# Kernel optimization log

Measured on AMD Instinct MI355X. Metric: run time of the kernel, lower is better.

Reference implementation:

```python
import itertools
import jax, jax.numpy as jnp
import numpy as np

B, O, E = 4096, 8, 64        # batch, num objects, latent dim
I, V = 4, 3                  # max_invariants, max_variables
PERM_IDXS = np.array(list(itertools.permutations(range(O), V)), dtype=np.int32)  # [P, V], P = 8*7*6 = 336


def setup_inputs() -> dict:
    key = jax.random.key(0)
    k1, k2, k3, k4 = jax.random.split(key, 4)
    return {
        "unary_feats": jax.random.normal(k1, (B, O, E), dtype=jnp.float32),
        "binary_feats": jax.random.normal(k2, (B, O, O, E), dtype=jnp.float32),
        # learned weights (RandomNormal(mean=0) in the original, stddev 0.05 default)
        "rule_unary": jax.random.normal(k3, (I, V, E), dtype=jnp.float32) * 0.05,
        "rule_binary": jax.random.normal(k4, (I, V, V, E), dtype=jnp.float32) * 0.05,
    }


def reference(unary_feats, binary_feats, rule_unary, rule_binary):
    perm = jnp.asarray(PERM_IDXS)  # [P, V]
    # unary_match[b,i,k,l] = sum_e unary_feats[b,l,e] * rule_unary[i,k,e]
    unary_match = jnp.einsum('ble,ike->bikl', unary_feats, rule_unary)  # [B, I, V, O]
    # gather: unary_perm_scores[b,i,p,v] = unary_match[b,i,v,perm[p,v]]
    v_idx = jnp.arange(V)[None, :]                      # [1, V]
    unary_perm_scores = unary_match[:, :, v_idx, perm]  # [B, I, P, V]
    unary_scores = unary_perm_scores.sum(-1)            # [B, I, P]

    # binary_match[b,i,n,m,j,k] = sum_e binary_feats[b,j,k,e] * rule_binary[i,n,m,e]
    binary_match = jnp.einsum('bjke,inme->binmjk', binary_feats, rule_binary)  # [B, I, V, V, O, O]
    # gather per permutation: scores[b,i,p,n,m] = binary_match[b,i,n,m,perm[p,n],perm[p,m]]
    n = jnp.arange(V)[None, :, None]  # [1, V, 1]
    m = jnp.arange(V)[None, None, :]  # [1, 1, V]
    pn = perm[:, :, None]             # [P, V, 1]
    pm = perm[:, None, :]             # [P, 1, V]
    binary_perm_scores = binary_match[:, :, n, m, pn, pm]  # [B, I, P, V, V]
    binary_scores = binary_perm_scores.sum((-1, -2))        # [B, I, P]

    merged_scores = (unary_scores + binary_scores).min(-1)  # [B, I] (min over permutations)
    inv_select = jax.nn.softmax(merged_scores, axis=-1)     # [B, I]
    rule_labels = jax.nn.one_hot(jnp.array([0, 0, 1, 1]), 4, dtype=inv_select.dtype)  # [4, 4]
    return inv_select @ rule_labels                          # [B, 4]
```

## Files before the change

kernel.cpp:

```cpp
#include <hip/hip_runtime.h>
#include <math.h>


typedef __attribute__((ext_vector_type(8))) __bf16 bf16x8;
typedef __attribute__((ext_vector_type(4))) float  f32x4;

#define BMS 68
#define QS3 68

__device__ inline bf16x8 cvt2(const float4 v0, const float4 v1) {
    bf16x8 r;
    r[0] = (__bf16)v0.x; r[1] = (__bf16)v0.y; r[2] = (__bf16)v0.z; r[3] = (__bf16)v0.w;
    r[4] = (__bf16)v1.x; r[5] = (__bf16)v1.y; r[6] = (__bf16)v1.z; r[7] = (__bf16)v1.w;
    return r;
}

__global__ __launch_bounds__(64, 2) void rule_learner_kernel(
    const float* __restrict__ uf,
    const float* __restrict__ bfe,
    const float* __restrict__ ru,
    const float* __restrict__ rb,
    float* __restrict__ out)
{
    const int b0    = blockIdx.x * 2;
    const int lane  = threadIdx.x;
    const int row16 = lane & 15;
    const int kg    = lane >> 4;
    const int kb    = kg * 8;

    __shared__ float bm[36 * BMS];
    __shared__ float um[12 * 12];
    __shared__ float q [12 * QS3];

    float4 af[4][4], uA[4];
    {
        const float* base = bfe + (size_t)b0 * 4096;
        #pragma unroll
        for (int t = 0; t < 4; ++t) {
            const float* rp = base + (size_t)(t * 16 + row16) * 64 + kb;
            af[t][0] = *(const float4*)rp;
            af[t][1] = *(const float4*)(rp + 4);
            af[t][2] = *(const float4*)(rp + 32);
            af[t][3] = *(const float4*)(rp + 36);
        }
        const float* up = uf + (size_t)b0 * 512 + (row16 < 8 ? row16 : 7) * 64 + kb;
        uA[0] = *(const float4*)up;
        uA[1] = *(const float4*)(up + 4);
        uA[2] = *(const float4*)(up + 32);
        uA[3] = *(const float4*)(up + 36);
    }

    bf16x8 rbf[6], ruf0, ruf1;
    {
        #pragma unroll
        for (int nt = 0; nt < 3; ++nt) {
            const int rule = nt * 16 + row16;
            const float* rp = rb + (rule < 36 ? rule : 35) * 64 + kb;
            rbf[nt * 2 + 0] = cvt2(*(const float4*)rp,        *(const float4*)(rp + 4));
            rbf[nt * 2 + 1] = cvt2(*(const float4*)(rp + 32), *(const float4*)(rp + 36));
        }
        const float* up = ru + (row16 < 12 ? row16 : 11) * 64 + kb;
        ruf0 = cvt2(*(const float4*)up,        *(const float4*)(up + 4));
        ruf1 = cvt2(*(const float4*)(up + 32), *(const float4*)(up + 36));
    }

    #pragma unroll
    for (int e = 0; e < 2; ++e) {
        #pragma unroll
        for (int t = 0; t < 4; ++t) {
            const bf16x8 a0 = cvt2(af[t][0], af[t][1]);
            const bf16x8 a1 = cvt2(af[t][2], af[t][3]);
            #pragma unroll
            for (int nt = 0; nt < 3; ++nt) {
                f32x4 acc = {0.f, 0.f, 0.f, 0.f};
                acc = __builtin_amdgcn_mfma_f32_16x16x32_bf16(a0, rbf[nt * 2 + 0], acc, 0, 0, 0);
                acc = __builtin_amdgcn_mfma_f32_16x16x32_bf16(a1, rbf[nt * 2 + 1], acc, 0, 0, 0);
                const int rule = nt * 16 + row16;
                if (rule < 36)
                    *(float4*)&bm[rule * BMS + t * 16 + kg * 4] = *(float4*)&acc;
            }
        }
        {
            const bf16x8 ua0 = cvt2(uA[0], uA[1]);
            const bf16x8 ua1 = cvt2(uA[2], uA[3]);
            f32x4 acc = {0.f, 0.f, 0.f, 0.f};
            acc = __builtin_amdgcn_mfma_f32_16x16x32_bf16(ua0, ruf0, acc, 0, 0, 0);
            acc = __builtin_amdgcn_mfma_f32_16x16x32_bf16(ua1, ruf1, acc, 0, 0, 0);
            if (row16 < 12 && kg < 2)
                *(float4*)&um[row16 * 12 + kg * 4] = *(float4*)&acc;
        }

        if (e == 0) {
            const float* base = bfe + (size_t)(b0 + 1) * 4096;
            #pragma unroll
            for (int t = 0; t < 4; ++t) {
                const float* rp = base + (size_t)(t * 16 + row16) * 64 + kb;
                af[t][0] = *(const float4*)rp;
                af[t][1] = *(const float4*)(rp + 4);
                af[t][2] = *(const float4*)(rp + 32);
                af[t][3] = *(const float4*)(rp + 36);
            }
            const float* up = uf + (size_t)(b0 + 1) * 512
                            + (row16 < 8 ? row16 : 7) * 64 + kb;
            uA[0] = *(const float4*)up;
            uA[1] = *(const float4*)(up + 4);
            uA[2] = *(const float4*)(up + 32);
            uA[3] = *(const float4*)(up + 36);
        }

        {
            const int x = lane >> 3;
            const int y = lane & 7;
            #pragma unroll
            for (int i = 0; i < 4; ++i) {
                const float* bmi = bm + i * 9 * BMS;
                const float* umi = um + i * 3 * 12;
                const float q01 = umi[x] + umi[12 + y]
                                + bmi[0 * BMS + x * 9] + bmi[4 * BMS + y * 9]
                                + bmi[1 * BMS + x * 8 + y] + bmi[3 * BMS + y * 8 + x];
                const float q02 = umi[24 + y] + bmi[8 * BMS + y * 9]
                                + bmi[2 * BMS + x * 8 + y] + bmi[6 * BMS + y * 8 + x];
                const float q12 = bmi[5 * BMS + x * 8 + y] + bmi[7 * BMS + y * 8 + x];
                q[(i * 3 + 0) * QS3 + lane] = q01;
                q[(i * 3 + 1) * QS3 + lane] = q02;
                q[(i * 3 + 2) * QS3 + lane] = q12;
            }
        }

        float mn[4] = {INFINITY, INFINITY, INFINITY, INFINITY};
        if (lane < 56) {
            const int a  = lane / 7;
            const int o  = lane - a * 7;
            const int bb = o + (o >= a);
            #pragma unroll
            for (int i = 0; i < 4; ++i) {
                const float bs  = q[(i * 3 + 0) * QS3 + a * 8 + bb];
                const float4 c0 = *(const float4*)&q[(i * 3 + 1) * QS3 + a * 8];
                const float4 c1 = *(const float4*)&q[(i * 3 + 1) * QS3 + a * 8 + 4];
                const float4 d0 = *(const float4*)&q[(i * 3 + 2) * QS3 + bb * 8];
                const float4 d1 = *(const float4*)&q[(i * 3 + 2) * QS3 + bb * 8 + 4];
                float vv[8];
                vv[0] = c0.x + d0.x; vv[1] = c0.y + d0.y;
                vv[2] = c0.z + d0.z; vv[3] = c0.w + d0.w;
                vv[4] = c1.x + d1.x; vv[5] = c1.y + d1.y;
                vv[6] = c1.z + d1.z; vv[7] = c1.w + d1.w;
                float m = INFINITY;
                #pragma unroll
                for (int cc = 0; cc < 8; ++cc) {
                    const float s = (cc == a || cc == bb) ? INFINITY : (bs + vv[cc]);
                    m = fminf(m, s);
                }
                mn[i] = m;
            }
        }
        #pragma unroll
        for (int s = 1; s <= 32; s <<= 1) {
            #pragma unroll
            for (int i = 0; i < 4; ++i) mn[i] = fminf(mn[i], __shfl_xor(mn[i], s));
        }
        if (lane == 0) {
            const float mx = fmaxf(fmaxf(mn[0], mn[1]), fmaxf(mn[2], mn[3]));
            const float e0 = expf(mn[0] - mx), e1 = expf(mn[1] - mx);
            const float e2 = expf(mn[2] - mx), e3 = expf(mn[3] - mx);
            const float inv = 1.f / (e0 + e1 + e2 + e3);
            *(float4*)(out + (size_t)(b0 + e) * 4) =
                make_float4((e0 + e1) * inv, (e2 + e3) * inv, 0.f, 0.f);
        }

        if (e == 0) {
            asm volatile("s_waitcnt lgkmcnt(0)" ::: "memory");
            __builtin_amdgcn_sched_barrier(0);
        }
    }
}

extern "C" void kernel_launch(void* const* d_in, const int* in_sizes, int n_in,
                              void* d_out, int out_size, void* d_ws, size_t ws_size,
                              hipStream_t stream) {
    const float* uf = (const float*)d_in[0];
    const float* bf = (const float*)d_in[1];
    const float* ru = (const float*)d_in[2];
    const float* rb = (const float*)d_in[3];
    float* out = (float*)d_out;

    const int B = in_sizes[0] / (8 * 64);
    rule_learner_kernel<<<B / 2, 64, 0, stream>>>(uf, bf, ru, rb, out);
}
```

Before: 20.66 us.

## Cut binary MFMAs by folding rule pairs and diagonal terms into fewer GEMMs

The kernel no longer computes all 36 rule-by-pair binary matches. It computes only the off-diagonal rule pairs needed for each (i,pair) slot, two rule sets of 12 columns each, and adds the transposed partner from shared memory. The diagonal binary terms are merged into the unary MFMA by loading the diagonal binary_feats rows. This reduces MFMA count and shared-memory traffic, and it drops the separate q-assembly pass, at the cost of extra diagonal loads and a strided transposed LDS gather.

```diff
diff --git a/kernel.cpp b/kernel.cpp
--- a/kernel.cpp
+++ b/kernel.cpp
@@ -5,8 +5,8 @@
 typedef __attribute__((ext_vector_type(8))) __bf16 bf16x8;
 typedef __attribute__((ext_vector_type(4))) float  f32x4;
 
-#define BMS 68
-#define QS3 68
+#define QS 68
+#define SS 12
 
 __device__ inline bf16x8 cvt2(const float4 v0, const float4 v1) {
     bf16x8 r;
@@ -28,11 +28,32 @@
     const int kg    = lane >> 4;
     const int kb    = kg * 8;
 
-    __shared__ float bm[36 * BMS];
-    __shared__ float um[12 * 12];
-    __shared__ float q [12 * QS3];
-
-    float4 af[4][4], uA[4];
+    __shared__ float q_s [12 * QS];
+    __shared__ float q2_s[12 * QS];
+    __shared__ float ss_s[12 * SS];
+
+    const int cc16  = row16 < 12 ? row16 : 11;
+    const int ii    = cc16 / 3, tt = cc16 - ii * 3;
+    const int rule1 = ii * 9 + (tt == 0 ? 1 : tt == 1 ? 2 : 5);
+    const int rule2 = ii * 9 + (tt == 0 ? 3 : tt == 1 ? 6 : 7);
+    const int ruled = ii * 9 + tt * 4;
+    bf16x8 b1f0, b1f1, b2f0, b2f1, dbf0, dbf1, ruf0, ruf1;
+    {
+        const float* r1 = rb + rule1 * 64 + kb;
+        b1f0 = cvt2(*(const float4*)r1,        *(const float4*)(r1 + 4));
+        b1f1 = cvt2(*(const float4*)(r1 + 32), *(const float4*)(r1 + 36));
+        const float* r2 = rb + rule2 * 64 + kb;
+        b2f0 = cvt2(*(const float4*)r2,        *(const float4*)(r2 + 4));
+        b2f1 = cvt2(*(const float4*)(r2 + 32), *(const float4*)(r2 + 36));
+        const float* rd = rb + ruled * 64 + kb;
+        dbf0 = cvt2(*(const float4*)rd,        *(const float4*)(rd + 4));
+        dbf1 = cvt2(*(const float4*)(rd + 32), *(const float4*)(rd + 36));
+        const float* rr = ru + cc16 * 64 + kb;
+        ruf0 = cvt2(*(const float4*)rr,        *(const float4*)(rr + 4));
+        ruf1 = cvt2(*(const float4*)(rr + 32), *(const float4*)(rr + 36));
+    }
+
+    float4 af[4][4], uA[4], dA[4];
     {
         const float* base = bfe + (size_t)b0 * 4096;
         #pragma unroll
@@ -43,51 +64,44 @@
             af[t][2] = *(const float4*)(rp + 32);
             af[t][3] = *(const float4*)(rp + 36);
         }
-        const float* up = uf + (size_t)b0 * 512 + (row16 < 8 ? row16 : 7) * 64 + kb;
-        uA[0] = *(const float4*)up;
-        uA[1] = *(const float4*)(up + 4);
-        uA[2] = *(const float4*)(up + 32);
-        uA[3] = *(const float4*)(up + 36);
-    }
-
-    bf16x8 rbf[6], ruf0, ruf1;
-    {
-        #pragma unroll
-        for (int nt = 0; nt < 3; ++nt) {
-            const int rule = nt * 16 + row16;
-            const float* rp = rb + (rule < 36 ? rule : 35) * 64 + kb;
-            rbf[nt * 2 + 0] = cvt2(*(const float4*)rp,        *(const float4*)(rp + 4));
-            rbf[nt * 2 + 1] = cvt2(*(const float4*)(rp + 32), *(const float4*)(rp + 36));
-        }
-        const float* up = ru + (row16 < 12 ? row16 : 11) * 64 + kb;
-        ruf0 = cvt2(*(const float4*)up,        *(const float4*)(up + 4));
-        ruf1 = cvt2(*(const float4*)(up + 32), *(const float4*)(up + 36));
+        const int v8c = row16 < 8 ? row16 : 7;
+        const float* up = uf + (size_t)b0 * 512 + v8c * 64 + kb;
+        uA[0] = *(const float4*)up;        uA[1] = *(const float4*)(up + 4);
+        uA[2] = *(const float4*)(up + 32); uA[3] = *(const float4*)(up + 36);
+        const float* dp = base + v8c * 576 + kb;
+        dA[0] = *(const float4*)dp;        dA[1] = *(const float4*)(dp + 4);
+        dA[2] = *(const float4*)(dp + 32); dA[3] = *(const float4*)(dp + 36);
     }
 
     #pragma unroll
     for (int e = 0; e < 2; ++e) {
+        f32x4 g1[4];
         #pragma unroll
         for (int t = 0; t < 4; ++t) {
             const bf16x8 a0 = cvt2(af[t][0], af[t][1]);
             const bf16x8 a1 = cvt2(af[t][2], af[t][3]);
-            #pragma unroll
-            for (int nt = 0; nt < 3; ++nt) {
-                f32x4 acc = {0.f, 0.f, 0.f, 0.f};
-                acc = __builtin_amdgcn_mfma_f32_16x16x32_bf16(a0, rbf[nt * 2 + 0], acc, 0, 0, 0);
-                acc = __builtin_amdgcn_mfma_f32_16x16x32_bf16(a1, rbf[nt * 2 + 1], acc, 0, 0, 0);
-                const int rule = nt * 16 + row16;
-                if (rule < 36)
-                    *(float4*)&bm[rule * BMS + t * 16 + kg * 4] = *(float4*)&acc;
-            }
+            f32x4 z1 = {0.f, 0.f, 0.f, 0.f};
+            z1 = __builtin_amdgcn_mfma_f32_16x16x32_bf16(a0, b1f0, z1, 0, 0, 0);
+            z1 = __builtin_amdgcn_mfma_f32_16x16x32_bf16(a1, b1f1, z1, 0, 0, 0);
+            g1[t] = z1;
+            f32x4 z2 = {0.f, 0.f, 0.f, 0.f};
+            z2 = __builtin_amdgcn_mfma_f32_16x16x32_bf16(a0, b2f0, z2, 0, 0, 0);
+            z2 = __builtin_amdgcn_mfma_f32_16x16x32_bf16(a1, b2f1, z2, 0, 0, 0);
+            if (row16 < 12)
+                *(float4*)&q2_s[row16 * QS + t * 16 + kg * 4] = *(float4*)&z2;
         }
         {
             const bf16x8 ua0 = cvt2(uA[0], uA[1]);
             const bf16x8 ua1 = cvt2(uA[2], uA[3]);
-            f32x4 acc = {0.f, 0.f, 0.f, 0.f};
-            acc = __builtin_amdgcn_mfma_f32_16x16x32_bf16(ua0, ruf0, acc, 0, 0, 0);
-            acc = __builtin_amdgcn_mfma_f32_16x16x32_bf16(ua1, ruf1, acc, 0, 0, 0);
+            const bf16x8 da0 = cvt2(dA[0], dA[1]);
+            const bf16x8 da1 = cvt2(dA[2], dA[3]);
+            f32x4 zs = {0.f, 0.f, 0.f, 0.f};
+            zs = __builtin_amdgcn_mfma_f32_16x16x32_bf16(ua0, ruf0, zs, 0, 0, 0);
+            zs = __builtin_amdgcn_mfma_f32_16x16x32_bf16(ua1, ruf1, zs, 0, 0, 0);
+            zs = __builtin_amdgcn_mfma_f32_16x16x32_bf16(da0, dbf0, zs, 0, 0, 0);
+            zs = __builtin_amdgcn_mfma_f32_16x16x32_bf16(da1, dbf1, zs, 0, 0, 0);
             if (row16 < 12 && kg < 2)
-                *(float4*)&um[row16 * 12 + kg * 4] = *(float4*)&acc;
+                *(float4*)&ss_s[row16 * SS + kg * 4] = *(float4*)&zs;
         }
 
         if (e == 0) {
@@ -100,30 +114,40 @@
                 af[t][2] = *(const float4*)(rp + 32);
                 af[t][3] = *(const float4*)(rp + 36);
             }
-            const float* up = uf + (size_t)(b0 + 1) * 512
-                            + (row16 < 8 ? row16 : 7) * 64 + kb;
-            uA[0] = *(const float4*)up;
-            uA[1] = *(const float4*)(up + 4);
-            uA[2] = *(const float4*)(up + 32);
-            uA[3] = *(const float4*)(up + 36);
-        }
-
-        {
-            const int x = lane >> 3;
-            const int y = lane & 7;
-            #pragma unroll
-            for (int i = 0; i < 4; ++i) {
-                const float* bmi = bm + i * 9 * BMS;
-                const float* umi = um + i * 3 * 12;
-                const float q01 = umi[x] + umi[12 + y]
-                                + bmi[0 * BMS + x * 9] + bmi[4 * BMS + y * 9]
-                                + bmi[1 * BMS + x * 8 + y] + bmi[3 * BMS + y * 8 + x];
-                const float q02 = umi[24 + y] + bmi[8 * BMS + y * 9]
-                                + bmi[2 * BMS + x * 8 + y] + bmi[6 * BMS + y * 8 + x];
-                const float q12 = bmi[5 * BMS + x * 8 + y] + bmi[7 * BMS + y * 8 + x];
-                q[(i * 3 + 0) * QS3 + lane] = q01;
-                q[(i * 3 + 1) * QS3 + lane] = q02;
-                q[(i * 3 + 2) * QS3 + lane] = q12;
+            const int v8c = row16 < 8 ? row16 : 7;
+            const float* up = uf + (size_t)(b0 + 1) * 512 + v8c * 64 + kb;
+            uA[0] = *(const float4*)up;        uA[1] = *(const float4*)(up + 4);
+            uA[2] = *(const float4*)(up + 32); uA[3] = *(const float4*)(up + 36);
+            const float* dp = base + v8c * 576 + kb;
+            dA[0] = *(const float4*)dp;        dA[1] = *(const float4*)(dp + 4);
+            dA[2] = *(const float4*)(dp + 32); dA[3] = *(const float4*)(dp + 36);
+        }
+
+        if (row16 < 12) {
+            #pragma unroll
+            for (int t = 0; t < 4; ++t) {
+                const int p0 = t * 16 + kg * 4;
+                float4 add;
+                {
+                    const int p = p0 + 0, rv = ((p & 7) << 3) | (p >> 3);
+                    add.x = q2_s[row16 * QS + rv];
+                }
+                {
+                    const int p = p0 + 1, rv = ((p & 7) << 3) | (p >> 3);
+                    add.y = q2_s[row16 * QS + rv];
+                }
+                {
+                    const int p = p0 + 2, rv = ((p & 7) << 3) | (p >> 3);
+                    add.z = q2_s[row16 * QS + rv];
+                }
+                {
+                    const int p = p0 + 3, rv = ((p & 7) << 3) | (p >> 3);
+                    add.w = q2_s[row16 * QS + rv];
+                }
+                float4 res;
+                res.x = g1[t][0] + add.x; res.y = g1[t][1] + add.y;
+                res.z = g1[t][2] + add.z; res.w = g1[t][3] + add.w;
+                *(float4*)&q_s[row16 * QS + p0] = res;
             }
         }
 
@@ -134,16 +158,20 @@
             const int bb = o + (o >= a);
             #pragma unroll
             for (int i = 0; i < 4; ++i) {
-                const float bs  = q[(i * 3 + 0) * QS3 + a * 8 + bb];
-                const float4 c0 = *(const float4*)&q[(i * 3 + 1) * QS3 + a * 8];
-                const float4 c1 = *(const float4*)&q[(i * 3 + 1) * QS3 + a * 8 + 4];
-                const float4 d0 = *(const float4*)&q[(i * 3 + 2) * QS3 + bb * 8];
-                const float4 d1 = *(const float4*)&q[(i * 3 + 2) * QS3 + bb * 8 + 4];
+                const float bs = q_s[(i * 3 + 0) * QS + a * 8 + bb]
+                               + ss_s[(i * 3 + 0) * SS + a]
+                               + ss_s[(i * 3 + 1) * SS + bb];
+                const float4 c0 = *(const float4*)&q_s[(i * 3 + 1) * QS + a * 8];
+                const float4 c1 = *(const float4*)&q_s[(i * 3 + 1) * QS + a * 8 + 4];
+                const float4 d0 = *(const float4*)&q_s[(i * 3 + 2) * QS + bb * 8];
+                const float4 d1 = *(const float4*)&q_s[(i * 3 + 2) * QS + bb * 8 + 4];
+                const float4 e0 = *(const float4*)&ss_s[(i * 3 + 2) * SS];
+                const float4 e1 = *(const float4*)&ss_s[(i * 3 + 2) * SS + 4];
                 float vv[8];
-                vv[0] = c0.x + d0.x; vv[1] = c0.y + d0.y;
-                vv[2] = c0.z + d0.z; vv[3] = c0.w + d0.w;
-                vv[4] = c1.x + d1.x; vv[5] = c1.y + d1.y;
-                vv[6] = c1.z + d1.z; vv[7] = c1.w + d1.w;
+                vv[0] = c0.x + d0.x + e0.x; vv[1] = c0.y + d0.y + e0.y;
+                vv[2] = c0.z + d0.z + e0.z; vv[3] = c0.w + d0.w + e0.w;
+                vv[4] = c1.x + d1.x + e1.x; vv[5] = c1.y + d1.y + e1.y;
+                vv[6] = c1.z + d1.z + e1.z; vv[7] = c1.w + d1.w + e1.w;
                 float m = INFINITY;
                 #pragma unroll
                 for (int cc = 0; cc < 8; ++cc) {
```

New measurement: 21.44 us. +3.8%, slower.

## Transpose binary match layout to pair-major and keep q01 in registers

Applied to the files above, without the earlier changes.

Swaps the MFMA operand order so binary match results are stored per object pair (64 rows) with rules permuted into a packed order. The q-assembly phase can then read contiguous float4/float2 vectors per lane instead of many scalar strided LDS loads. The q01 term stays in registers rather than going through shared memory, and the min phase uses all 64 lanes indexed directly by (x,y). The gain relies on getting the rule permutation and the LDS strides right, and there is a risk of LDS bank conflicts with the new stride of 52.

```diff
diff --git a/kernel.cpp b/kernel.cpp
--- a/kernel.cpp
+++ b/kernel.cpp
@@ -5,8 +5,9 @@
 typedef __attribute__((ext_vector_type(8))) __bf16 bf16x8;
 typedef __attribute__((ext_vector_type(4))) float  f32x4;
 
-#define BMS 68
-#define QS3 68
+#define BMS2 52
+#define QS2  68
+#define SSU  12
 
 __device__ inline bf16x8 cvt2(const float4 v0, const float4 v1) {
     bf16x8 r;
@@ -27,10 +28,30 @@
     const int row16 = lane & 15;
     const int kg    = lane >> 4;
     const int kb    = kg * 8;
+    const int x     = lane >> 3;
+    const int y     = lane & 7;
+    const int rev   = y * 8 + x;
 
-    __shared__ float bm[36 * BMS];
-    __shared__ float um[12 * 12];
-    __shared__ float q [12 * QS3];
+    __shared__ float bm_t[64 * BMS2];
+    __shared__ float q_s [8 * QS2];
+    __shared__ float um  [12 * SSU];
+
+    bf16x8 raf[6];
+    #pragma unroll
+    for (int T = 0; T < 3; ++T) {
+        const int c = T * 16 + row16;
+        const int i = c / 12, s = c - i * 12;
+        const int m = (int)((0x008407630521ull >> (4 * s)) & 15ull);
+        const float* rp = rb + (i * 9 + m) * 64 + kb;
+        raf[T * 2 + 0] = cvt2(*(const float4*)rp,        *(const float4*)(rp + 4));
+        raf[T * 2 + 1] = cvt2(*(const float4*)(rp + 32), *(const float4*)(rp + 36));
+    }
+    bf16x8 ruf0, ruf1;
+    {
+        const float* rr = ru + (row16 < 12 ? row16 : 11) * 64 + kb;
+        ruf0 = cvt2(*(const float4*)rr,        *(const float4*)(rr + 4));
+        ruf1 = cvt2(*(const float4*)(rr + 32), *(const float4*)(rr + 36));
+    }
 
     float4 af[4][4], uA[4];
     {
@@ -44,40 +65,22 @@
             af[t][3] = *(const float4*)(rp + 36);
         }
         const float* up = uf + (size_t)b0 * 512 + (row16 < 8 ? row16 : 7) * 64 + kb;
-        uA[0] = *(const float4*)up;
-        uA[1] = *(const float4*)(up + 4);
-        uA[2] = *(const float4*)(up + 32);
-        uA[3] = *(const float4*)(up + 36);
-    }
-
-    bf16x8 rbf[6], ruf0, ruf1;
-    {
-        #pragma unroll
-        for (int nt = 0; nt < 3; ++nt) {
-            const int rule = nt * 16 + row16;
-            const float* rp = rb + (rule < 36 ? rule : 35) * 64 + kb;
-            rbf[nt * 2 + 0] = cvt2(*(const float4*)rp,        *(const float4*)(rp + 4));
-            rbf[nt * 2 + 1] = cvt2(*(const float4*)(rp + 32), *(const float4*)(rp + 36));
-        }
-        const float* up = ru + (row16 < 12 ? row16 : 11) * 64 + kb;
-        ruf0 = cvt2(*(const float4*)up,        *(const float4*)(up + 4));
-        ruf1 = cvt2(*(const float4*)(up + 32), *(const float4*)(up + 36));
+        uA[0] = *(const float4*)up;        uA[1] = *(const float4*)(up + 4);
+        uA[2] = *(const float4*)(up + 32); uA[3] = *(const float4*)(up + 36);
     }
 
     #pragma unroll
-    for (int e = 0; e < 2; ++e) {
+    for (int el = 0; el < 2; ++el) {
         #pragma unroll
-        for (int t = 0; t < 4; ++t) {
-            const bf16x8 a0 = cvt2(af[t][0], af[t][1]);
-            const bf16x8 a1 = cvt2(af[t][2], af[t][3]);
+        for (int P = 0; P < 4; ++P) {
+            const bf16x8 fb0 = cvt2(af[P][0], af[P][1]);
+            const bf16x8 fb1 = cvt2(af[P][2], af[P][3]);
             #pragma unroll
-            for (int nt = 0; nt < 3; ++nt) {
+            for (int T = 0; T < 3; ++T) {
                 f32x4 acc = {0.f, 0.f, 0.f, 0.f};
-                acc = __builtin_amdgcn_mfma_f32_16x16x32_bf16(a0, rbf[nt * 2 + 0], acc, 0, 0, 0);
-                acc = __builtin_amdgcn_mfma_f32_16x16x32_bf16(a1, rbf[nt * 2 + 1], acc, 0, 0, 0);
-                const int rule = nt * 16 + row16;
-                if (rule < 36)
-                    *(float4*)&bm[rule * BMS + t * 16 + kg * 4] = *(float4*)&acc;
+                acc = __builtin_amdgcn_mfma_f32_16x16x32_bf16(raf[T * 2 + 0], fb0, acc, 0, 0, 0);
+                acc = __builtin_amdgcn_mfma_f32_16x16x32_bf16(raf[T * 2 + 1], fb1, acc, 0, 0, 0);
+                *(float4*)&bm_t[(P * 16 + row16) * BMS2 + T * 16 + kg * 4] = *(float4*)&acc;
             }
         }
         {
@@ -87,14 +90,14 @@
             acc = __builtin_amdgcn_mfma_f32_16x16x32_bf16(ua0, ruf0, acc, 0, 0, 0);
             acc = __builtin_amdgcn_mfma_f32_16x16x32_bf16(ua1, ruf1, acc, 0, 0, 0);
             if (row16 < 12 && kg < 2)
-                *(float4*)&um[row16 * 12 + kg * 4] = *(float4*)&acc;
+                *(float4*)&um[row16 * SSU + kg * 4] = *(float4*)&acc;
         }
 
-        if (e == 0) {
-            const float* base = bfe + (size_t)(b0 + 1) * 4096;
+        if (el == 0) {
+            const float* nb = bfe + (size_t)(b0 + 1) * 4096;
             #pragma unroll
             for (int t = 0; t < 4; ++t) {
-                const float* rp = base + (size_t)(t * 16 + row16) * 64 + kb;
+                const float* rp = nb + (size_t)(t * 16 + row16) * 64 + kb;
                 af[t][0] = *(const float4*)rp;
                 af[t][1] = *(const float4*)(rp + 4);
                 af[t][2] = *(const float4*)(rp + 32);
@@ -102,43 +105,34 @@
             }
             const float* up = uf + (size_t)(b0 + 1) * 512
                             + (row16 < 8 ? row16 : 7) * 64 + kb;
-            uA[0] = *(const float4*)up;
-            uA[1] = *(const float4*)(up + 4);
-            uA[2] = *(const float4*)(up + 32);
-            uA[3] = *(const float4*)(up + 36);
+            uA[0] = *(const float4*)up;        uA[1] = *(const float4*)(up + 4);
+            uA[2] = *(const float4*)(up + 32); uA[3] = *(const float4*)(up + 36);
         }
 
-        {
-            const int x = lane >> 3;
-            const int y = lane & 7;
-            #pragma unroll
-            for (int i = 0; i < 4; ++i) {
-                const float* bmi = bm + i * 9 * BMS;
-                const float* umi = um + i * 3 * 12;
-                const float q01 = umi[x] + umi[12 + y]
-                                + bmi[0 * BMS + x * 9] + bmi[4 * BMS + y * 9]
-                                + bmi[1 * BMS + x * 8 + y] + bmi[3 * BMS + y * 8 + x];
-                const float q02 = umi[24 + y] + bmi[8 * BMS + y * 9]
-                                + bmi[2 * BMS + x * 8 + y] + bmi[6 * BMS + y * 8 + x];
-                const float q12 = bmi[5 * BMS + x * 8 + y] + bmi[7 * BMS + y * 8 + x];
-                q[(i * 3 + 0) * QS3 + lane] = q01;
-                q[(i * 3 + 1) * QS3 + lane] = q02;
-                q[(i * 3 + 2) * QS3 + lane] = q12;
-            }
+        float q01r[4];
+        #pragma unroll
+        for (int i = 0; i < 4; ++i) {
+            const float4 F = *(const float4*)&bm_t[lane * BMS2 + i * 12];
+            const float4 R = *(const float4*)&bm_t[rev  * BMS2 + i * 12 + 4];
+            const float2 D = *(const float2*)&bm_t[(y * 9) * BMS2 + i * 12 + 8];
+            const float  z = bm_t[(x * 9) * BMS2 + i * 12 + 3];
+            const float u0 = um[(i * 3 + 0) * SSU + x];
+            const float u1 = um[(i * 3 + 1) * SSU + y];
+            const float u2 = um[(i * 3 + 2) * SSU + y];
+            q01r[i] = F.x + R.x + z + D.x + u0 + u1;
+            q_s[(i * 2 + 0) * QS2 + lane] = F.y + R.y + D.y + u2;
+            q_s[(i * 2 + 1) * QS2 + lane] = F.z + R.z;
         }
 
         float mn[4] = {INFINITY, INFINITY, INFINITY, INFINITY};
-        if (lane < 56) {
-            const int a  = lane / 7;
-            const int o  = lane - a * 7;
-            const int bb = o + (o >= a);
+        if (x != y) {
             #pragma unroll
             for (int i = 0; i < 4; ++i) {
-                const float bs  = q[(i * 3 + 0) * QS3 + a * 8 + bb];
-                const float4 c0 = *(const float4*)&q[(i * 3 + 1) * QS3 + a * 8];
-                const float4 c1 = *(const float4*)&q[(i * 3 + 1) * QS3 + a * 8 + 4];
-                const float4 d0 = *(const float4*)&q[(i * 3 + 2) * QS3 + bb * 8];
-                const float4 d1 = *(const float4*)&q[(i * 3 + 2) * QS3 + bb * 8 + 4];
+                const float  bs = q01r[i];
+                const float4 c0 = *(const float4*)&q_s[(i * 2 + 0) * QS2 + x * 8];
+                const float4 c1 = *(const float4*)&q_s[(i * 2 + 0) * QS2 + x * 8 + 4];
+                const float4 d0 = *(const float4*)&q_s[(i * 2 + 1) * QS2 + y * 8];
+                const float4 d1 = *(const float4*)&q_s[(i * 2 + 1) * QS2 + y * 8 + 4];
                 float vv[8];
                 vv[0] = c0.x + d0.x; vv[1] = c0.y + d0.y;
                 vv[2] = c0.z + d0.z; vv[3] = c0.w + d0.w;
@@ -147,7 +141,7 @@
                 float m = INFINITY;
                 #pragma unroll
                 for (int cc = 0; cc < 8; ++cc) {
-                    const float s = (cc == a || cc == bb) ? INFINITY : (bs + vv[cc]);
+                    const float s = (cc == x || cc == y) ? INFINITY : (bs + vv[cc]);
                     m = fminf(m, s);
                 }
                 mn[i] = m;
@@ -163,11 +157,11 @@
             const float e0 = expf(mn[0] - mx), e1 = expf(mn[1] - mx);
             const float e2 = expf(mn[2] - mx), e3 = expf(mn[3] - mx);
             const float inv = 1.f / (e0 + e1 + e2 + e3);
-            *(float4*)(out + (size_t)(b0 + e) * 4) =
+            *(float4*)(out + (size_t)(b0 + el) * 4) =
                 make_float4((e0 + e1) * inv, (e2 + e3) * inv, 0.f, 0.f);
         }
 
-        if (e == 0) {
+        if (el == 0) {
             asm volatile("s_waitcnt lgkmcnt(0)" ::: "memory");
             __builtin_amdgcn_sched_barrier(0);
         }
```

Measured after the change: 21.16 us. 2.5% more time.

## Process one batch per block and raise occupancy instead of manual prefetch

Applied to the files above, without the earlier changes.

Each block now handles a single batch element instead of two, so the grid doubles and the manual software prefetch of the second element goes away. Occupancy is raised by moving launch_bounds from 2 to 4 and by converting loaded inputs to bf16 immediately, which cuts live registers. Shared memory is shrunk by aliasing the q buffer onto the bm buffer and tightening the row strides. The aim is to hide the latency of the memory-bound binary-feature loads with more resident waves rather than explicit double-buffering. The cost is some extra per-block overhead, and the shared-memory aliasing is only safe because the kernel runs as a single wave.

```diff
diff --git a/kernel.cpp b/kernel.cpp
--- a/kernel.cpp
+++ b/kernel.cpp
@@ -5,8 +5,8 @@
 typedef __attribute__((ext_vector_type(8))) __bf16 bf16x8;
 typedef __attribute__((ext_vector_type(4))) float  f32x4;
 
-#define BMS 68
-#define QS3 68
+#define BMS 66
+#define SSU 12
 
 __device__ inline bf16x8 cvt2(const float4 v0, const float4 v1) {
     bf16x8 r;
@@ -15,39 +15,36 @@
     return r;
 }
 
-__global__ __launch_bounds__(64, 2) void rule_learner_kernel(
+__global__ __launch_bounds__(64, 4) void rule_learner_kernel(
     const float* __restrict__ uf,
     const float* __restrict__ bfe,
     const float* __restrict__ ru,
     const float* __restrict__ rb,
     float* __restrict__ out)
 {
-    const int b0    = blockIdx.x * 2;
+    const int b     = blockIdx.x;
     const int lane  = threadIdx.x;
     const int row16 = lane & 15;
     const int kg    = lane >> 4;
     const int kb    = kg * 8;
 
-    __shared__ float bm[36 * BMS];
-    __shared__ float um[12 * 12];
-    __shared__ float q [12 * QS3];
+    __shared__ float smem[36 * BMS + 12 * SSU];
+    float* bm = smem;
+    float* qq = smem;
+    float* um = smem + 36 * BMS;
 
-    float4 af[4][4], uA[4];
+    bf16x8 a0[4], a1[4], ua0, ua1;
     {
-        const float* base = bfe + (size_t)b0 * 4096;
+        const float* base = bfe + (size_t)b * 4096;
         #pragma unroll
         for (int t = 0; t < 4; ++t) {
             const float* rp = base + (size_t)(t * 16 + row16) * 64 + kb;
-            af[t][0] = *(const float4*)rp;
-            af[t][1] = *(const float4*)(rp + 4);
-            af[t][2] = *(const float4*)(rp + 32);
-            af[t][3] = *(const float4*)(rp + 36);
+            a0[t] = cvt2(*(const float4*)rp,        *(const float4*)(rp + 4));
+            a1[t] = cvt2(*(const float4*)(rp + 32), *(const float4*)(rp + 36));
         }
-        const float* up = uf + (size_t)b0 * 512 + (row16 < 8 ? row16 : 7) * 64 + kb;
-        uA[0] = *(const float4*)up;
-        uA[1] = *(const float4*)(up + 4);
-        uA[2] = *(const float4*)(up + 32);
-        uA[3] = *(const float4*)(up + 36);
+        const float* up = uf + (size_t)b * 512 + (row16 < 8 ? row16 : 7) * 64 + kb;
+        ua0 = cvt2(*(const float4*)up,        *(const float4*)(up + 4));
+        ua1 = cvt2(*(const float4*)(up + 32), *(const float4*)(up + 36));
     }
 
     bf16x8 rbf[6], ruf0, ruf1;
@@ -65,112 +62,83 @@
     }
 
     #pragma unroll
-    for (int e = 0; e < 2; ++e) {
+    for (int t = 0; t < 4; ++t) {
         #pragma unroll
-        for (int t = 0; t < 4; ++t) {
-            const bf16x8 a0 = cvt2(af[t][0], af[t][1]);
-            const bf16x8 a1 = cvt2(af[t][2], af[t][3]);
+        for (int nt = 0; nt < 3; ++nt) {
+            f32x4 acc = {0.f, 0.f, 0.f, 0.f};
+            acc = __builtin_amdgcn_mfma_f32_16x16x32_bf16(a0[t], rbf[nt * 2 + 0], acc, 0, 0, 0);
+            acc = __builtin_amdgcn_mfma_f32_16x16x32_bf16(a1[t], rbf[nt * 2 + 1], acc, 0, 0, 0);
+            const int rule = nt * 16 + row16;
+            if (rule < 36)
+                *(float4*)&bm[rule * BMS + t * 16 + kg * 4] = *(float4*)&acc;
+        }
+    }
+    {
+        f32x4 acc = {0.f, 0.f, 0.f, 0.f};
+        acc = __builtin_amdgcn_mfma_f32_16x16x32_bf16(ua0, ruf0, acc, 0, 0, 0);
+        acc = __builtin_amdgcn_mfma_f32_16x16x32_bf16(ua1, ruf1, acc, 0, 0, 0);
+        if (row16 < 12 && kg < 2)
+            *(float4*)&um[row16 * SSU + kg * 4] = *(float4*)&acc;
+    }
+
+    {
+        const int x = lane >> 3;
+        const int y = lane & 7;
+        #pragma unroll
+        for (int i = 0; i < 4; ++i) {
+            const float* bmi = bm + i * 9 * BMS;
+            const float* umi = um + i * 3 * SSU;
+            const float q01 = umi[x] + umi[SSU + y]
+                            + bmi[0 * BMS + x * 9] + bmi[4 * BMS + y * 9]
+                            + bmi[1 * BMS + x * 8 + y] + bmi[3 * BMS + y * 8 + x];
+            const float q02 = umi[2 * SSU + y] + bmi[8 * BMS + y * 9]
+                            + bmi[2 * BMS + x * 8 + y] + bmi[6 * BMS + y * 8 + x];
+            const float q12 = bmi[5 * BMS + x * 8 + y] + bmi[7 * BMS + y * 8 + x];
+            qq[(i * 3 + 0) * BMS + lane] = q01;
+            qq[(i * 3 + 1) * BMS + lane] = q02;
+            qq[(i * 3 + 2) * BMS + lane] = q12;
+        }
+    }
+
+    float mn[4] = {INFINITY, INFINITY, INFINITY, INFINITY};
+    if (lane < 56) {
+        const int a  = lane / 7;
+        const int o  = lane - a * 7;
+        const int bb = o + (o >= a);
+        #pragma unroll
+        for (int i = 0; i < 4; ++i) {
+            const float bs  = qq[(i * 3 + 0) * BMS + a * 8 + bb];
+            const float4 c0 = *(const float4*)&qq[(i * 3 + 1) * BMS + a * 8];
+            const float4 c1 = *(const float4*)&qq[(i * 3 + 1) * BMS + a * 8 + 4];
+            const float4 d0 = *(const float4*)&qq[(i * 3 + 2) * BMS + bb * 8];
+            const float4 d1 = *(const float4*)&qq[(i * 3 + 2) * BMS + bb * 8 + 4];
+            float vv[8];
+            vv[0] = c0.x + d0.x; vv[1] = c0.y + d0.y;
+            vv[2] = c0.z + d0.z; vv[3] = c0.w + d0.w;
+            vv[4] = c1.x + d1.x; vv[5] = c1.y + d1.y;
+            vv[6] = c1.z + d1.z; vv[7] = c1.w + d1.w;
+            float m = INFINITY;
             #pragma unroll
-            for (int nt = 0; nt < 3; ++nt) {
-                f32x4 acc = {0.f, 0.f, 0.f, 0.f};
-                acc = __builtin_amdgcn_mfma_f32_16x16x32_bf16(a0, rbf[nt * 2 + 0], acc, 0, 0, 0);
-                acc = __builtin_amdgcn_mfma_f32_16x16x32_bf16(a1, rbf[nt * 2 + 1], acc, 0, 0, 0);
-                const int rule = nt * 16 + row16;
-                if (rule < 36)
-                    *(float4*)&bm[rule * BMS + t * 16 + kg * 4] = *(float4*)&acc;
+            for (int cc = 0; cc < 8; ++cc) {
+                const float s = (cc == a || cc == bb) ? INFINITY : (bs + vv[cc]);
+                m = fminf(m, s);
             }
+            mn[i] = m;
         }
-        {
-            const bf16x8 ua0 = cvt2(uA[0], uA[1]);
-            const bf16x8 ua1 = cvt2(uA[2], uA[3]);
-            f32x4 acc = {0.f, 0.f, 0.f, 0.f};
-            acc = __builtin_amdgcn_mfma_f32_16x16x32_bf16(ua0, ruf0, acc, 0, 0, 0);
-            acc = __builtin_amdgcn_mfma_f32_16x16x32_bf16(ua1, ruf1, acc, 0, 0, 0);
-            if (row16 < 12 && kg < 2)
-                *(float4*)&um[row16 * 12 + kg * 4] = *(float4*)&acc;
-        }
+    }
+    #pragma unroll
+    for (int s = 1; s <= 32; s <<= 1) {
+        #pragma unroll
+        for (int i = 0; i < 4; ++i) mn[i] = fminf(mn[i], __shfl_xor(mn[i], s));
+    }
 
-        if (e == 0) {
-            const float* base = bfe + (size_t)(b0 + 1) * 4096;
-            #pragma unroll
-            for (int t = 0; t < 4; ++t) {
-                const float* rp = base + (size_t)(t * 16 + row16) * 64 + kb;
-                af[t][0] = *(const float4*)rp;
-                af[t][1] = *(const float4*)(rp + 4);
-                af[t][2] = *(const float4*)(rp + 32);
-                af[t][3] = *(const float4*)(rp + 36);
-            }
-            const float* up = uf + (size_t)(b0 + 1) * 512
-                            + (row16 < 8 ? row16 : 7) * 64 + kb;
-            uA[0] = *(const float4*)up;
-            uA[1] = *(const float4*)(up + 4);
-            uA[2] = *(const float4*)(up + 32);
-            uA[3] = *(const float4*)(up + 36);
-        }
-
-        {
-            const int x = lane >> 3;
-            const int y = lane & 7;
-            #pragma unroll
-            for (int i = 0; i < 4; ++i) {
-                const float* bmi = bm + i * 9 * BMS;
-                const float* umi = um + i * 3 * 12;
-                const float q01 = umi[x] + umi[12 + y]
-                                + bmi[0 * BMS + x * 9] + bmi[4 * BMS + y * 9]
-                                + bmi[1 * BMS + x * 8 + y] + bmi[3 * BMS + y * 8 + x];
-                const float q02 = umi[24 + y] + bmi[8 * BMS + y * 9]
-                                + bmi[2 * BMS + x * 8 + y] + bmi[6 * BMS + y * 8 + x];
-                const float q12 = bmi[5 * BMS + x * 8 + y] + bmi[7 * BMS + y * 8 + x];
-                q[(i * 3 + 0) * QS3 + lane] = q01;
-                q[(i * 3 + 1) * QS3 + lane] = q02;
-                q[(i * 3 + 2) * QS3 + lane] = q12;
-            }
-        }
-
-        float mn[4] = {INFINITY, INFINITY, INFINITY, INFINITY};
-        if (lane < 56) {
-            const int a  = lane / 7;
-            const int o  = lane - a * 7;
-            const int bb = o + (o >= a);
-            #pragma unroll
-            for (int i = 0; i < 4; ++i) {
-                const float bs  = q[(i * 3 + 0) * QS3 + a * 8 + bb];
-                const float4 c0 = *(const float4*)&q[(i * 3 + 1) * QS3 + a * 8];
-                const float4 c1 = *(const float4*)&q[(i * 3 + 1) * QS3 + a * 8 + 4];
-                const float4 d0 = *(const float4*)&q[(i * 3 + 2) * QS3 + bb * 8];
-                const float4 d1 = *(const float4*)&q[(i * 3 + 2) * QS3 + bb * 8 + 4];
-                float vv[8];
-                vv[0] = c0.x + d0.x; vv[1] = c0.y + d0.y;
-                vv[2] = c0.z + d0.z; vv[3] = c0.w + d0.w;
-                vv[4] = c1.x + d1.x; vv[5] = c1.y + d1.y;
-                vv[6] = c1.z + d1.z; vv[7] = c1.w + d1.w;
-                float m = INFINITY;
-                #pragma unroll
-                for (int cc = 0; cc < 8; ++cc) {
-                    const float s = (cc == a || cc == bb) ? INFINITY : (bs + vv[cc]);
-                    m = fminf(m, s);
-                }
-                mn[i] = m;
-            }
-        }
-        #pragma unroll
-        for (int s = 1; s <= 32; s <<= 1) {
-            #pragma unroll
-            for (int i = 0; i < 4; ++i) mn[i] = fminf(mn[i], __shfl_xor(mn[i], s));
-        }
-        if (lane == 0) {
-            const float mx = fmaxf(fmaxf(mn[0], mn[1]), fmaxf(mn[2], mn[3]));
-            const float e0 = expf(mn[0] - mx), e1 = expf(mn[1] - mx);
-            const float e2 = expf(mn[2] - mx), e3 = expf(mn[3] - mx);
-            const float inv = 1.f / (e0 + e1 + e2 + e3);
-            *(float4*)(out + (size_t)(b0 + e) * 4) =
-                make_float4((e0 + e1) * inv, (e2 + e3) * inv, 0.f, 0.f);
-        }
-
-        if (e == 0) {
-            asm volatile("s_waitcnt lgkmcnt(0)" ::: "memory");
-            __builtin_amdgcn_sched_barrier(0);
-        }
+    if (lane == 0) {
+        const float mx = fmaxf(fmaxf(mn[0], mn[1]), fmaxf(mn[2], mn[3]));
+        const float e0 = expf(mn[0] - mx), e1 = expf(mn[1] - mx);
+        const float e2 = expf(mn[2] - mx), e3 = expf(mn[3] - mx);
+        const float inv = 1.f / (e0 + e1 + e2 + e3);
+        *(float4*)(out + (size_t)b * 4) =
+            make_float4((e0 + e1) * inv, (e2 + e3) * inv, 0.f, 0.f);
     }
 }
 
@@ -184,5 +152,5 @@
     float* out = (float*)d_out;
 
     const int B = in_sizes[0] / (8 * 64);
-    rule_learner_kernel<<<B / 2, 64, 0, stream>>>(uf, bf, ru, rb, out);
+    rule_learner_kernel<<<B, 64, 0, stream>>>(uf, bf, ru, rb, out);
 }
```

After: 28.82 us. 39.5% more time.
